# Kernel optimization log

Measured on AMD Instinct MI355X. Metric: run time of the kernel, lower is better.

Reference implementation:

```python
import jax, jax.numpy as jnp
import numpy as np

N_NODES = 100000
N_EDGES = 1000000
D_FEAT = 64
QMAX = 127.0  # signed int8 symmetric fake-quant (Degree-Quant low-precision path)


def _degree_quant(x, protect_mask):
    """Degree-Quant stage: protected (mask=True) rows stay full precision
    ('high' quantizer = identity); unprotected rows are fake-quantized to
    signed int8 with a dynamic per-tensor scale computed over the
    unprotected subset only (matching msg[~mask] -> quant_low in torch),
    using a straight-through estimator."""
    m = protect_mask[:, None]  # [R,1] broadcast over features
    low = jnp.logical_not(m)
    amax = jnp.max(jnp.where(low, jnp.abs(x), 0.0))
    scale = jnp.maximum(amax / QMAX, jnp.float32(1e-8))
    q = jnp.clip(jnp.round(x / scale), -QMAX - 1.0, QMAX) * scale
    q_ste = x + jax.lax.stop_gradient(q - x)  # STE: identity gradient
    return jnp.where(m, x, q_ste)


def setup_inputs() -> dict:
    key = jax.random.key(0)
    k1, k2, k3 = jax.random.split(key, 3)
    x = jax.random.normal(k1, (N_NODES, D_FEAT), dtype=jnp.float32)
    edge_index = jax.random.randint(k2, (2, N_EDGES), 0, N_NODES, dtype=jnp.int32)
    mask = jax.random.randint(k3, (N_NODES,), 0, 2, dtype=jnp.int32).astype(jnp.bool_)
    return {"x": x, "edge_index": edge_index, "mask": mask}


def reference(x, edge_index, mask):
    # flow='source_to_target': j=0 (source), i=1 (target)
    src = edge_index[0]
    dst = edge_index[1]
    # __collect__: x_j = x.index_select(0, edge_index[0])  -> [E, D] gather
    msg = x[src]
    # training path: edge_mask = mask[edge_index[0]]; high/low message quant
    edge_mask = mask[src]
    msg_q = _degree_quant(msg, edge_mask)
    # aggregate: scatter-add over target index with dim_size = N
    aggr = jax.ops.segment_sum(msg_q, dst, num_segments=N_NODES)
    # node-level high/low quant after aggregation
    aggr_q = _degree_quant(aggr, mask)
    # update() is identity, followed by another node-level high/low quant
    out = _degree_quant(aggr_q, mask)
    return out
```

## Files before the change

kernel.cpp:

```cpp
#include <hip/hip_runtime.h>
#include <hip/hip_bf16.h>
#include <stdint.h>

#define N_NODES 100000
#define N_EDGES 1000000
#define D_FEAT  64
#define QMAX    127.0f

#define BSHIFT      6
#define NODES_PER_B 64
#define NBUCK       1563
#define BCAP        960
#define A_EBLK      4096
#define A_THREADS   512
#define A_NBLK      ((N_EDGES + A_EBLK - 1) / A_EBLK)
#define B_THREADS   256

struct Scalars {
    unsigned int layout_flag;
    unsigned int amax_msg;
    unsigned int pad[2];
};

__device__ __forceinline__ bool get_mask(const void* mp, unsigned int flag, int i) {
    if (flag & 2u) return ((const float*)mp)[i] != 0.0f;
    if (flag & 1u) return ((const unsigned char*)mp)[i] != 0;
    return ((const int*)mp)[i] != 0;
}

__device__ __forceinline__ float wave_max(float v) {
    #pragma unroll
    for (int o = 32; o > 0; o >>= 1) v = fmaxf(v, __shfl_xor(v, o, 64));
    return v;
}

__device__ __forceinline__ float dq(float x, float scale) {
    float t = rintf(x / scale);
    t = fminf(fmaxf(t, -QMAX - 1.0f), QMAX);
    return t * scale;
}

__device__ __forceinline__ unsigned short f2b(float f) {
    unsigned int u = __float_as_uint(f);
    u += 0x7FFFu + ((u >> 16) & 1u);
    return (unsigned short)(u >> 16);
}
__device__ __forceinline__ float b2f_lo(unsigned int w) {
    return __uint_as_float(w << 16);
}
__device__ __forceinline__ float b2f_hi(unsigned int w) {
    return __uint_as_float(w & 0xFFFF0000u);
}

__global__ void detect_kernel(const unsigned int* mw, Scalars* sc) {
    unsigned int f = 0;
    for (int i = blockIdx.x * blockDim.x + threadIdx.x; i < N_NODES / 4;
         i += gridDim.x * blockDim.x) {
        unsigned int w = mw[i];
        if (w == 0x3F800000u) f |= 2u;
        else if (w & 0xFFFFFF00u) f |= 1u;
    }
    if (f) atomicOr(&sc->layout_flag, f);
}

__global__ void rowmax_amax_kernel(const float4* __restrict__ x4,
                                   const void* maskp, Scalars* sc) {
    __shared__ float smx[4];
    unsigned int flag = sc->layout_flag;
    int t = threadIdx.x;
    int gtid = blockIdx.x * blockDim.x + t;
    int row = gtid >> 4, sub = gtid & 15;
    float v = 0.0f;
    if (row < N_NODES && !get_mask(maskp, flag, row)) {
        float4 a = x4[row * 16 + sub];
        v = fmaxf(fmaxf(fabsf(a.x), fabsf(a.y)), fmaxf(fabsf(a.z), fabsf(a.w)));
    }
    v = wave_max(v);
    if ((t & 63) == 0) smx[t >> 6] = v;
    __syncthreads();
    if (t == 0) {
        v = fmaxf(fmaxf(smx[0], smx[1]), fmaxf(smx[2], smx[3]));
        if (v > __uint_as_float(*(volatile unsigned int*)&sc->amax_msg))
            atomicMax(&sc->amax_msg, __float_as_uint(v));
    }
}

__global__ void bucket_kernel(const int* __restrict__ src, const int* __restrict__ dst,
                              int* __restrict__ gcur, unsigned int* __restrict__ region) {
    __shared__ int hist[NBUCK];
    __shared__ int dlds[A_EBLK];
    int t = threadIdx.x;
    for (int i = t; i < NBUCK; i += A_THREADS) hist[i] = 0;
    __syncthreads();
    int beg = blockIdx.x * A_EBLK;
    int end = beg + A_EBLK; if (end > N_EDGES) end = N_EDGES;
    for (int e = beg + t; e < end; e += A_THREADS) {
        int d = dst[e];
        dlds[e - beg] = d;
        atomicAdd(&hist[d >> BSHIFT], 1);
    }
    __syncthreads();
    for (int i = t; i < NBUCK; i += A_THREADS) {
        int h = hist[i];
        hist[i] = h ? atomicAdd(&gcur[i], h) : 0;
    }
    __syncthreads();
    for (int e = beg + t; e < end; e += A_THREADS) {
        int s = src[e], d = dlds[e - beg];
        int b = d >> BSHIFT;
        int pos = atomicAdd(&hist[b], 1);
        if (pos < BCAP)
            region[b * BCAP + pos] =
                (unsigned)s | ((unsigned)(d & (NODES_PER_B - 1)) << 17);
    }
}

__global__ void msg_quant_kernel(const float4* __restrict__ x4, const void* maskp,
                                 const Scalars* __restrict__ sc,
                                 uint4* __restrict__ msgu4) {
    int i8 = blockIdx.x * blockDim.x + threadIdx.x;
    const int total8 = N_NODES * 8;
    if (i8 >= total8) return;
    unsigned int flag = sc->layout_flag;
    float scale = fmaxf(__uint_as_float(sc->amax_msg) / QMAX, 1e-8f);
    float4 a = x4[i8 * 2];
    float4 b = x4[i8 * 2 + 1];
    if (!get_mask(maskp, flag, i8 >> 3)) {
        a.x = dq(a.x, scale); a.y = dq(a.y, scale);
        a.z = dq(a.z, scale); a.w = dq(a.w, scale);
        b.x = dq(b.x, scale); b.y = dq(b.y, scale);
        b.z = dq(b.z, scale); b.w = dq(b.w, scale);
    }
    uint4 u;
    u.x = (unsigned)f2b(a.x) | ((unsigned)f2b(a.y) << 16);
    u.y = (unsigned)f2b(a.z) | ((unsigned)f2b(a.w) << 16);
    u.z = (unsigned)f2b(b.x) | ((unsigned)f2b(b.y) << 16);
    u.w = (unsigned)f2b(b.z) | ((unsigned)f2b(b.w) << 16);
    msgu4[i8] = u;
}

#define AGG_SORT_PROLOGUE                                                     \
    __shared__ unsigned int pk[BCAP];                                         \
    __shared__ unsigned int srt[BCAP];                                        \
    __shared__ int cnt0[NODES_PER_B];                                         \
    __shared__ int scn[NODES_PER_B];                                          \
    __shared__ int cur[NODES_PER_B];                                          \
    __shared__ float smx[B_THREADS / 64];                                     \
    int b = blockIdx.x;                                                       \
    int t = threadIdx.x;                                                      \
    int ne = gcur[b]; if (ne > BCAP) ne = BCAP;                               \
    if (t < NODES_PER_B) cnt0[t] = 0;                                         \
    __syncthreads();                                                          \
    for (int i = t; i < ne; i += B_THREADS) {                                 \
        unsigned int w = region[b * BCAP + i];                                \
        pk[i] = w;                                                            \
        atomicAdd(&cnt0[(w >> 17) & (NODES_PER_B - 1)], 1);                   \
    }                                                                         \
    __syncthreads();                                                          \
    if (t < NODES_PER_B) scn[t] = cnt0[t];                                    \
    __syncthreads();                                                          \
    for (int o = 1; o < NODES_PER_B; o <<= 1) {                               \
        int add = 0;                                                          \
        if (t < NODES_PER_B && t >= o) add = scn[t - o];                      \
        __syncthreads();                                                      \
        if (t < NODES_PER_B) scn[t] += add;                                   \
        __syncthreads();                                                      \
    }                                                                         \
    if (t < NODES_PER_B) cur[t] = scn[t] - cnt0[t];                           \
    __syncthreads();                                                          \
    for (int i = t; i < ne; i += B_THREADS) {                                 \
        unsigned int w = pk[i];                                               \
        int pos = atomicAdd(&cur[(w >> 17) & (NODES_PER_B - 1)], 1);          \
        srt[pos] = w & 0x1FFFFu;                                              \
    }                                                                         \
    __syncthreads();

#define AGG_EPILOGUE                                                          \
    vmax = wave_max(vmax);                                                    \
    if ((t & 63) == 0) smx[t >> 6] = vmax;                                    \
    __syncthreads();                                                          \
    if (t == 0) {                                                             \
        float v = smx[0];                                                     \
        _Pragma("unroll")                                                     \
        for (int k = 1; k < B_THREADS / 64; ++k) v = fmaxf(v, smx[k]);        \
        pmax[b] = v;                                                          \
    }

__global__ void aggregate_fast_kernel(const uint4* __restrict__ msgu4,
                                      const unsigned int* __restrict__ region,
                                      const int* __restrict__ gcur,
                                      const void* maskp,
                                      const Scalars* __restrict__ sc,
                                      float4* __restrict__ out4,
                                      float* __restrict__ pmax) {
    unsigned int flag = sc->layout_flag;
    AGG_SORT_PROLOGUE
    int grp = t >> 3, sub = t & 7;
    float vmax = 0.0f;
    #pragma unroll
    for (int k = 0; k < 2; ++k) {
        int n = grp + 32 * k;
        int node = b * NODES_PER_B + n;
        if (node >= N_NODES) continue;
        int e1 = scn[n], e0 = e1 - cnt0[n];
        float s0 = 0.f, s1 = 0.f, s2 = 0.f, s3 = 0.f;
        float s4 = 0.f, s5 = 0.f, s6 = 0.f, s7 = 0.f;
        int e = e0;
        for (; e + 3 < e1; e += 4) {
            uint4 u0 = msgu4[srt[e]     * 8 + sub];
            uint4 u1 = msgu4[srt[e + 1] * 8 + sub];
            uint4 u2 = msgu4[srt[e + 2] * 8 + sub];
            uint4 u3 = msgu4[srt[e + 3] * 8 + sub];
            s0 += (b2f_lo(u0.x) + b2f_lo(u1.x)) + (b2f_lo(u2.x) + b2f_lo(u3.x));
            s1 += (b2f_hi(u0.x) + b2f_hi(u1.x)) + (b2f_hi(u2.x) + b2f_hi(u3.x));
            s2 += (b2f_lo(u0.y) + b2f_lo(u1.y)) + (b2f_lo(u2.y) + b2f_lo(u3.y));
            s3 += (b2f_hi(u0.y) + b2f_hi(u1.y)) + (b2f_hi(u2.y) + b2f_hi(u3.y));
            s4 += (b2f_lo(u0.z) + b2f_lo(u1.z)) + (b2f_lo(u2.z) + b2f_lo(u3.z));
            s5 += (b2f_hi(u0.z) + b2f_hi(u1.z)) + (b2f_hi(u2.z) + b2f_hi(u3.z));
            s6 += (b2f_lo(u0.w) + b2f_lo(u1.w)) + (b2f_lo(u2.w) + b2f_lo(u3.w));
            s7 += (b2f_hi(u0.w) + b2f_hi(u1.w)) + (b2f_hi(u2.w) + b2f_hi(u3.w));
        }
        for (; e < e1; ++e) {
            uint4 u = msgu4[srt[e] * 8 + sub];
            s0 += b2f_lo(u.x); s1 += b2f_hi(u.x);
            s2 += b2f_lo(u.y); s3 += b2f_hi(u.y);
            s4 += b2f_lo(u.z); s5 += b2f_hi(u.z);
            s6 += b2f_lo(u.w); s7 += b2f_hi(u.w);
        }
        float4 oa = make_float4(s0, s1, s2, s3);
        float4 ob = make_float4(s4, s5, s6, s7);
        out4[node * 16 + sub * 2]     = oa;
        out4[node * 16 + sub * 2 + 1] = ob;
        if (!get_mask(maskp, flag, node)) {
            float m = fmaxf(fmaxf(fmaxf(fabsf(s0), fabsf(s1)),
                                  fmaxf(fabsf(s2), fabsf(s3))),
                            fmaxf(fmaxf(fabsf(s4), fabsf(s5)),
                                  fmaxf(fabsf(s6), fabsf(s7))));
            vmax = fmaxf(vmax, m);
        }
    }
    AGG_EPILOGUE
}

__global__ void aggregate_q_kernel(const float4* __restrict__ x4,
                                   const unsigned int* __restrict__ region,
                                   const int* __restrict__ gcur,
                                   const void* maskp,
                                   const Scalars* __restrict__ sc,
                                   float4* __restrict__ out4,
                                   float* __restrict__ pmax) {
    unsigned int flag = sc->layout_flag;
    AGG_SORT_PROLOGUE
    float scale = fmaxf(__uint_as_float(sc->amax_msg) / QMAX, 1e-8f);
    int grp = t >> 4, sub = t & 15;
    float vmax = 0.0f;
    for (int n = grp; n < NODES_PER_B; n += 16) {
        int node = b * NODES_PER_B + n;
        if (node >= N_NODES) break;
        int e1 = scn[n], e0 = e1 - cnt0[n];
        float4 acc = {0.f, 0.f, 0.f, 0.f};
        for (int e = e0; e < e1; ++e) {
            int s = srt[e];
            float4 a = x4[s * 16 + sub];
            if (!get_mask(maskp, flag, s)) {
                a.x = dq(a.x, scale); a.y = dq(a.y, scale);
                a.z = dq(a.z, scale); a.w = dq(a.w, scale);
            }
            acc.x += a.x; acc.y += a.y; acc.z += a.z; acc.w += a.w;
        }
        out4[node * 16 + sub] = acc;
        if (!get_mask(maskp, flag, node))
            vmax = fmaxf(vmax, fmaxf(fmaxf(fabsf(acc.x), fabsf(acc.y)),
                                     fmaxf(fabsf(acc.z), fabsf(acc.w))));
    }
    AGG_EPILOGUE
}

__global__ void final_kernel(float4* __restrict__ aggr, const void* maskp,
                             const Scalars* __restrict__ sc,
                             const float* __restrict__ pmax) {
    __shared__ float sred[4];
    unsigned int flag = sc->layout_flag;
    int t = threadIdx.x;
    float v = 0.0f;
    for (int i = t; i < NBUCK; i += 256) v = fmaxf(v, pmax[i]);
    v = wave_max(v);
    if ((t & 63) == 0) sred[t >> 6] = v;
    __syncthreads();
    float amax1 = fmaxf(fmaxf(sred[0], sred[1]), fmaxf(sred[2], sred[3]));
    float s1 = fmaxf(amax1 / QMAX, 1e-8f);
    const int total4 = N_NODES * (D_FEAT / 4);
    for (int i = blockIdx.x * blockDim.x + t; i < total4;
         i += gridDim.x * blockDim.x) {
        int row = i >> 4;
        if (get_mask(maskp, flag, row)) continue;
        float4 a = aggr[i];
        a.x = dq(a.x, s1); a.y = dq(a.y, s1);
        a.z = dq(a.z, s1); a.w = dq(a.w, s1);
        aggr[i] = a;
    }
}

extern "C" void kernel_launch(void* const* d_in, const int* in_sizes, int n_in,
                              void* d_out, int out_size, void* d_ws, size_t ws_size,
                              hipStream_t stream) {
    const float* x    = (const float*)d_in[0];
    const int*   ei   = (const int*)d_in[1];
    const void*  mask = d_in[2];
    const int* src = ei;
    const int* dst = ei + N_EDGES;

    char* ws = (char*)d_ws;
    Scalars* sc   = (Scalars*)(ws + 0);
    int*   gcur   = (int*)    (ws + 256);
    float* pmax   = (float*)  (ws + 6528);
    uint4* msgb   = (uint4*)  (ws + 12800);
    const size_t REGION_FAST  = 12812800;
    const size_t REGION_BYTES = (size_t)NBUCK * BCAP * 4;
    bool fast = ws_size >= REGION_FAST + REGION_BYTES;
    unsigned int* region = (unsigned int*)(ws + (fast ? REGION_FAST : 12800));

    hipMemsetAsync(ws, 0, 6528, stream);

    detect_kernel<<<98, 256, 0, stream>>>((const unsigned int*)mask, sc);

    rowmax_amax_kernel<<<N_NODES * 16 / 256, 256, 0, stream>>>(
        (const float4*)x, mask, sc);

    bucket_kernel<<<A_NBLK, A_THREADS, 0, stream>>>(src, dst, gcur, region);

    if (fast) {
        const int total8 = N_NODES * 8;
        msg_quant_kernel<<<(total8 + 255) / 256, 256, 0, stream>>>(
            (const float4*)x, mask, sc, msgb);
        aggregate_fast_kernel<<<NBUCK, B_THREADS, 0, stream>>>(
            msgb, region, gcur, mask, sc, (float4*)d_out, pmax);
    } else {
        aggregate_q_kernel<<<NBUCK, B_THREADS, 0, stream>>>(
            (const float4*)x, region, gcur, mask, sc, (float4*)d_out, pmax);
    }

    final_kernel<<<2048, 256, 0, stream>>>((float4*)d_out, mask, sc, pmax);
}
```

Measured before the change: 95.94 us.

## Merge memset with mask detection and fuse bucketing with row-max into one launch

Replaces the hipMemsetAsync and the detect kernel with a single kernel that zeroes the scalar/counter workspace and detects the mask layout from only the first 4096 words. The bucket and row-max amax kernels are merged into one launch whose block index picks the role, so the two independent passes run concurrently. The msg_quant block size is raised to 512. This removes two launches and their gaps, but the layout detection now samples only a prefix of the mask, which could misclassify unusual mask encodings.

Result: faster. 77.92 us, median of 2 (-18.8%).

```diff
diff --git a/kernel.cpp b/kernel.cpp
--- a/kernel.cpp
+++ b/kernel.cpp
@@ -15,6 +15,10 @@
 #define A_THREADS   512
 #define A_NBLK      ((N_EDGES + A_EBLK - 1) / A_EBLK)
 #define B_THREADS   256
+#define ZERO_WORDS  1632
+#define DET_WORDS   4096
+#define RM_NBLK     (N_NODES * 16 / 512)
+#define K2_NBLK     (A_NBLK + RM_NBLK)
 
 struct Scalars {
     unsigned int layout_flag;
@@ -52,23 +56,67 @@
     return __uint_as_float(w & 0xFFFF0000u);
 }
 
-__global__ void detect_kernel(const unsigned int* mw, Scalars* sc) {
+__global__ void zero_detect_kernel(unsigned int* w, const unsigned int* mw) {
+    int t = threadIdx.x;
+    if (blockIdx.x < 7) {
+        int i = 1 + blockIdx.x * 256 + t;
+        if (i < ZERO_WORDS) w[i] = 0;
+        return;
+    }
+    __shared__ unsigned int sfl[4];
     unsigned int f = 0;
-    for (int i = blockIdx.x * blockDim.x + threadIdx.x; i < N_NODES / 4;
-         i += gridDim.x * blockDim.x) {
-        unsigned int w = mw[i];
-        if (w == 0x3F800000u) f |= 2u;
-        else if (w & 0xFFFFFF00u) f |= 1u;
-    }
-    if (f) atomicOr(&sc->layout_flag, f);
-}
-
-__global__ void rowmax_amax_kernel(const float4* __restrict__ x4,
-                                   const void* maskp, Scalars* sc) {
-    __shared__ float smx[4];
-    unsigned int flag = sc->layout_flag;
+    #pragma unroll
+    for (int k = 0; k < DET_WORDS / 256; ++k) {
+        unsigned int v = mw[k * 256 + t];
+        if (v == 0x3F800000u) f |= 2u;
+        else if (v & 0xFFFFFF00u) f |= 1u;
+    }
+    #pragma unroll
+    for (int o = 32; o > 0; o >>= 1) f |= __shfl_xor(f, o, 64);
+    if ((t & 63) == 0) sfl[t >> 6] = f;
+    __syncthreads();
+    if (t == 0) w[0] = sfl[0] | sfl[1] | sfl[2] | sfl[3];
+}
+
+__global__ __launch_bounds__(512)
+void bucket_rowmax_kernel(const int* __restrict__ src, const int* __restrict__ dst,
+                          int* __restrict__ gcur, unsigned int* __restrict__ region,
+                          const float4* __restrict__ x4, const void* maskp,
+                          Scalars* sc) {
+    __shared__ int hist[NBUCK];
+    __shared__ int dlds[A_EBLK];
+    __shared__ float smx[8];
     int t = threadIdx.x;
-    int gtid = blockIdx.x * blockDim.x + t;
+
+    if (blockIdx.x < A_NBLK) {
+        for (int i = t; i < NBUCK; i += A_THREADS) hist[i] = 0;
+        __syncthreads();
+        int beg = blockIdx.x * A_EBLK;
+        int end = beg + A_EBLK; if (end > N_EDGES) end = N_EDGES;
+        for (int e = beg + t; e < end; e += A_THREADS) {
+            int d = dst[e];
+            dlds[e - beg] = d;
+            atomicAdd(&hist[d >> BSHIFT], 1);
+        }
+        __syncthreads();
+        for (int i = t; i < NBUCK; i += A_THREADS) {
+            int h = hist[i];
+            hist[i] = h ? atomicAdd(&gcur[i], h) : 0;
+        }
+        __syncthreads();
+        for (int e = beg + t; e < end; e += A_THREADS) {
+            int s = src[e], d = dlds[e - beg];
+            int b = d >> BSHIFT;
+            int pos = atomicAdd(&hist[b], 1);
+            if (pos < BCAP)
+                region[b * BCAP + pos] =
+                    (unsigned)s | ((unsigned)(d & (NODES_PER_B - 1)) << 17);
+        }
+        return;
+    }
+
+    unsigned int flag = sc->layout_flag;
+    int gtid = (blockIdx.x - A_NBLK) * 512 + t;
     int row = gtid >> 4, sub = gtid & 15;
     float v = 0.0f;
     if (row < N_NODES && !get_mask(maskp, flag, row)) {
@@ -79,45 +127,16 @@
     if ((t & 63) == 0) smx[t >> 6] = v;
     __syncthreads();
     if (t == 0) {
-        v = fmaxf(fmaxf(smx[0], smx[1]), fmaxf(smx[2], smx[3]));
+        #pragma unroll
+        for (int k = 1; k < 8; ++k) v = fmaxf(v, smx[k]);
         if (v > __uint_as_float(*(volatile unsigned int*)&sc->amax_msg))
             atomicMax(&sc->amax_msg, __float_as_uint(v));
     }
 }
 
-__global__ void bucket_kernel(const int* __restrict__ src, const int* __restrict__ dst,
-                              int* __restrict__ gcur, unsigned int* __restrict__ region) {
-    __shared__ int hist[NBUCK];
-    __shared__ int dlds[A_EBLK];
-    int t = threadIdx.x;
-    for (int i = t; i < NBUCK; i += A_THREADS) hist[i] = 0;
-    __syncthreads();
-    int beg = blockIdx.x * A_EBLK;
-    int end = beg + A_EBLK; if (end > N_EDGES) end = N_EDGES;
-    for (int e = beg + t; e < end; e += A_THREADS) {
-        int d = dst[e];
-        dlds[e - beg] = d;
-        atomicAdd(&hist[d >> BSHIFT], 1);
-    }
-    __syncthreads();
-    for (int i = t; i < NBUCK; i += A_THREADS) {
-        int h = hist[i];
-        hist[i] = h ? atomicAdd(&gcur[i], h) : 0;
-    }
-    __syncthreads();
-    for (int e = beg + t; e < end; e += A_THREADS) {
-        int s = src[e], d = dlds[e - beg];
-        int b = d >> BSHIFT;
-        int pos = atomicAdd(&hist[b], 1);
-        if (pos < BCAP)
-            region[b * BCAP + pos] =
-                (unsigned)s | ((unsigned)(d & (NODES_PER_B - 1)) << 17);
-    }
-}
-
-__global__ void msg_quant_kernel(const float4* __restrict__ x4, const void* maskp,
-                                 const Scalars* __restrict__ sc,
-                                 uint4* __restrict__ msgu4) {
+__global__ __launch_bounds__(512)
+void msg_quant_kernel(const float4* __restrict__ x4, const void* maskp,
+                      const Scalars* __restrict__ sc, uint4* __restrict__ msgu4) {
     int i8 = blockIdx.x * blockDim.x + threadIdx.x;
     const int total8 = N_NODES * 8;
     if (i8 >= total8) return;
@@ -227,10 +246,8 @@
             s4 += b2f_lo(u.z); s5 += b2f_hi(u.z);
             s6 += b2f_lo(u.w); s7 += b2f_hi(u.w);
         }
-        float4 oa = make_float4(s0, s1, s2, s3);
-        float4 ob = make_float4(s4, s5, s6, s7);
-        out4[node * 16 + sub * 2]     = oa;
-        out4[node * 16 + sub * 2 + 1] = ob;
+        out4[node * 16 + sub * 2]     = make_float4(s0, s1, s2, s3);
+        out4[node * 16 + sub * 2 + 1] = make_float4(s4, s5, s6, s7);
         if (!get_mask(maskp, flag, node)) {
             float m = fmaxf(fmaxf(fmaxf(fabsf(s0), fabsf(s1)),
                                   fmaxf(fabsf(s2), fabsf(s3))),
@@ -320,18 +337,15 @@
     bool fast = ws_size >= REGION_FAST + REGION_BYTES;
     unsigned int* region = (unsigned int*)(ws + (fast ? REGION_FAST : 12800));
 
-    hipMemsetAsync(ws, 0, 6528, stream);
-
-    detect_kernel<<<98, 256, 0, stream>>>((const unsigned int*)mask, sc);
-
-    rowmax_amax_kernel<<<N_NODES * 16 / 256, 256, 0, stream>>>(
-        (const float4*)x, mask, sc);
-
-    bucket_kernel<<<A_NBLK, A_THREADS, 0, stream>>>(src, dst, gcur, region);
+    zero_detect_kernel<<<8, 256, 0, stream>>>((unsigned int*)ws,
+                                              (const unsigned int*)mask);
+
+    bucket_rowmax_kernel<<<K2_NBLK, 512, 0, stream>>>(
+        src, dst, gcur, region, (const float4*)x, mask, sc);
 
     if (fast) {
         const int total8 = N_NODES * 8;
-        msg_quant_kernel<<<(total8 + 255) / 256, 256, 0, stream>>>(
+        msg_quant_kernel<<<(total8 + 511) / 512, 512, 0, stream>>>(
             (const float4*)x, mask, sc, msgb);
         aggregate_fast_kernel<<<NBUCK, B_THREADS, 0, stream>>>(
             msgb, region, gcur, mask, sc, (float4*)d_out, pmax);
```
